# Kernel tuning notes

Measured on AMD Instinct MI355X. Metric: run time of the kernel, lower is better.

Reference implementation:

```python
import jax, jax.numpy as jnp
import numpy as np
from jax import lax

B = 16384
H = 1024   # h_dim
Z = 64     # z_dim
N = 2 * Z  # FFT length


def sample_von_mises(key, loc, kappa, rounds=32):
    """Best-Fisher rejection sampler for von Mises, vectorized, fixed rounds.
    Matches torch.distributions.VonMises.sample (non-differentiable)."""
    tau = 1.0 + jnp.sqrt(1.0 + 4.0 * kappa * kappa)
    rho = (tau - jnp.sqrt(2.0 * tau)) / (2.0 * kappa)
    r = (1.0 + rho * rho) / (2.0 * rho)

    def body(carry, k):
        theta, done = carry
        u = jax.random.uniform(k, (3,) + loc.shape, dtype=loc.dtype)
        u1, u2, u3 = u[0], u[1], u[2]
        zc = jnp.cos(jnp.pi * u1)
        f = (1.0 + r * zc) / (r + zc)
        c = kappa * (r - f)
        accept = ((c * (2.0 - c) - u2) > 0) | ((jnp.log(c / u2) + 1.0 - c) >= 0)
        prop = jnp.sign(u3 - 0.5) * jnp.arccos(jnp.clip(f, -1.0, 1.0))
        theta = jnp.where((~done) & accept, prop, theta)
        return (theta, done | accept), None

    init = (jnp.zeros_like(loc), jnp.zeros(loc.shape, bool))
    (theta, _), _ = lax.scan(body, init, jax.random.split(key, rounds))
    # shift by loc and wrap to [-pi, pi]
    return jnp.mod(theta + loc + jnp.pi, 2.0 * jnp.pi) - jnp.pi


def setup_inputs() -> dict:
    key = jax.random.key(0)
    ks = jax.random.split(key, 16)

    def lin(k, fan_in, fan_out):
        kw, kb = jax.random.split(k)
        bound = 1.0 / np.sqrt(fan_in)
        w = jax.random.uniform(kw, (fan_in, fan_out), jnp.float32, -bound, bound)
        b = jax.random.uniform(kb, (fan_out,), jnp.float32, -bound, bound)
        return w, b

    x = jax.random.uniform(ks[0], (B, 784), jnp.float32)
    enc_w1, enc_b1 = lin(ks[1], 784, 2 * H)
    enc_w2, enc_b2 = lin(ks[2], 2 * H, H)
    mu_w, mu_b = lin(ks[3], H, Z)
    conc_w, conc_b = lin(ks[4], H, 1)
    pre_w, pre_b = lin(ks[5], 4 * Z, Z)
    dec_w1, dec_b1 = lin(ks[6], Z, H)
    dec_w2, dec_b2 = lin(ks[7], H, 2 * H)
    dec_w3, dec_b3 = lin(ks[8], 2 * H, 784)
    return dict(x=x, enc_w1=enc_w1, enc_b1=enc_b1, enc_w2=enc_w2, enc_b2=enc_b2,
                mu_w=mu_w, mu_b=mu_b, conc_w=conc_w, conc_b=conc_b,
                pre_w=pre_w, pre_b=pre_b,
                dec_w1=dec_w1, dec_b1=dec_b1, dec_w2=dec_w2, dec_b2=dec_b2,
                dec_w3=dec_w3, dec_b3=dec_b3)


def reference(x, enc_w1, enc_b1, enc_w2, enc_b2, mu_w, mu_b, conc_w, conc_b,
              pre_w, pre_b, dec_w1, dec_b1, dec_w2, dec_b2, dec_w3, dec_b3):
    # ---- encode ----
    h = jax.nn.relu(x.reshape(-1, 784) @ enc_w1 + enc_b1)
    h = jax.nn.relu(h @ enc_w2 + enc_b2)
    mu = h @ mu_w + mu_b                                       # [B, Z]
    kappa = jax.nn.softplus(h @ conc_w + conc_b) + 1.0          # [B, 1]

    # ---- reparameterize: von Mises per-dim sampling (non-differentiable) ----
    kappa_full = jnp.broadcast_to(kappa, mu.shape)
    theta = sample_von_mises(jax.random.key(42),
                             lax.stop_gradient(mu),
                             lax.stop_gradient(kappa_full))     # [B, Z]
    theta = lax.stop_gradient(theta)

    # conjugate-symmetric phase spectrum: indices 0 and N/2 stay zero
    b = theta.shape[0]
    theta_s = jnp.zeros((b, N), theta.dtype)
    theta_s = theta_s.at[:, 1:Z].set(theta[:, 1:])
    theta_s = theta_s.at[:, N - Z + 1:].set(-theta[:, 1:][:, ::-1])

    z_c = jnp.fft.ifft(jnp.exp(1j * theta_s), axis=-1, norm='ortho')  # [B, N] complex
    # torch.view_as_real -> interleaved (re, im) pairs, flattened to [B, 4Z]
    z_real = jnp.stack([z_c.real, z_c.imag], axis=-1).reshape(b, -1).astype(jnp.float32)
    z = z_real @ pre_w + pre_b                                   # [B, Z]

    # ---- decode ----
    d = jax.nn.relu(z @ dec_w1 + dec_b1)
    d = jax.nn.relu(d @ dec_w2 + dec_b2)
    x_recon = d @ dec_w3 + dec_b3                                # [B, 784]
    return mu, kappa, z, x_recon
```

## Files before the change

kernel.cpp:

```cpp
#include <hip/hip_runtime.h>
#include <hip/hip_bf16.h>
#include <stdint.h>

#pragma clang fp contract(off)

#define PI_F     3.14159265358979323846f
#define TWO_PI_F 6.28318530717958647692f

typedef short short8 __attribute__((ext_vector_type(8)));
typedef float f32x4  __attribute__((ext_vector_type(4)));

__device__ __forceinline__ void tfround(uint32_t &x0, uint32_t &x1, const int r) {
  x0 += x1;
  x1 = (x1 << r) | (x1 >> (32 - r));
  x1 ^= x0;
}
__device__ __forceinline__ void threefry2x32(uint32_t k0, uint32_t k1,
                                             uint32_t &x0, uint32_t &x1) {
  uint32_t k2 = k0 ^ k1 ^ 0x1BD11BDAu;
  x0 += k0; x1 += k1;
  tfround(x0,x1,13); tfround(x0,x1,15); tfround(x0,x1,26); tfround(x0,x1,6);
  x0 += k1; x1 += k2 + 1u;
  tfround(x0,x1,17); tfround(x0,x1,29); tfround(x0,x1,16); tfround(x0,x1,24);
  x0 += k2; x1 += k0 + 2u;
  tfround(x0,x1,13); tfround(x0,x1,15); tfround(x0,x1,26); tfround(x0,x1,6);
  x0 += k0; x1 += k1 + 3u;
  tfround(x0,x1,17); tfround(x0,x1,29); tfround(x0,x1,16); tfround(x0,x1,24);
  x0 += k1; x1 += k2 + 4u;
  tfround(x0,x1,13); tfround(x0,x1,15); tfround(x0,x1,26); tfround(x0,x1,6);
  x0 += k2; x1 += k0 + 5u;
}
__device__ __forceinline__ float u01(uint32_t bits) {
  return __uint_as_float((bits >> 9) | 0x3F800000u) - 1.0f;
}
__global__ __launch_bounds__(64) void setup_keys(uint32_t* keys) {
  int r = threadIdx.x;
  if (r < 32) {
    uint32_t x0 = 0u, x1 = (uint32_t)r;
    threefry2x32(0u, 42u, x0, x1);
    keys[2 * r]     = x0;
    keys[2 * r + 1] = x1;
  }
}

__device__ __forceinline__ unsigned short bf16_rn(float v) {
  uint32_t u = __float_as_uint(v);
  return (unsigned short)((u + 0x7FFFu + ((u >> 16) & 1u)) >> 16);
}
__device__ __forceinline__ void split_bf16(float v, short &h, short &l) {
  unsigned short hb = bf16_rn(v);
  h = (short)hb;
  float hf = __uint_as_float(((uint32_t)hb) << 16);
  l = (short)bf16_rn(v - hf);
}

__global__ __launch_bounds__(256)
void split_pad(const float* __restrict__ src, short* __restrict__ dh,
               short* __restrict__ dl, int C, int Cp) {
  int r = blockIdx.x;
  for (int c = threadIdx.x; c < Cp; c += blockDim.x) {
    float v = (c < C) ? src[(size_t)r * C + c] : 0.0f;
    short h, l; split_bf16(v, h, l);
    dh[(size_t)r * Cp + c] = h;
    dl[(size_t)r * Cp + c] = l;
  }
}

__global__ __launch_bounds__(256)
void transpose_split(const float* __restrict__ src, short* __restrict__ dh,
                     short* __restrict__ dl, int K, int N, int Kp, int Np) {
  __shared__ float tile[32][33];
  int n0 = blockIdx.x * 32, k0 = blockIdx.y * 32;
  int tn = threadIdx.x & 31, tk4 = threadIdx.x >> 5;
  #pragma unroll
  for (int i = 0; i < 4; ++i) {
    int k = k0 + tk4 * 4 + i;
    float v = (k < K && (n0 + tn) < N) ? src[(size_t)k * N + n0 + tn] : 0.0f;
    tile[tk4 * 4 + i][tn] = v;
  }
  __syncthreads();
  #pragma unroll
  for (int i = 0; i < 4; ++i) {
    int n = n0 + tk4 * 4 + i;
    int k = k0 + tn;
    if (n < Np && k < Kp) {
      float v = tile[tn][tk4 * 4 + i];
      short h, l; split_bf16(v, h, l);
      dh[(size_t)n * Kp + k] = h;
      dl[(size_t)n * Kp + k] = l;
    }
  }
}

__device__ __forceinline__ void async16(void* l, const void* g) {
  __builtin_amdgcn_global_load_lds(
      (const __attribute__((address_space(1))) void*)(uintptr_t)g,
      (__attribute__((address_space(3))) void*)(uint32_t)(uintptr_t)l,
      16, 0, 0);
}

template<int RELU, int OUTMODE>
__global__ __launch_bounds__(256)
void gemm_mfma3(const short* __restrict__ Ah, const short* __restrict__ Al,
                const short* __restrict__ Bh, const short* __restrict__ Bl,
                const float* __restrict__ bias,
                float* __restrict__ Cf, short* __restrict__ Ch, short* __restrict__ Cl,
                int Kp, int NK, int Nout) {
  __shared__ short8 lds8[2048];

  int gx = gridDim.x;
  int nwg = gx * gridDim.y;
  int bid = blockIdx.y * gx + blockIdx.x;
  int cpx = nwg >> 3;
  int swz = (bid & 7) * cpx + (bid >> 3);
  int tile_x = swz % gx, tile_y = swz / gx;

  const int row0 = tile_y * 128;
  const int col0 = tile_x * 128;
  const int t = threadIdx.x;
  const int lane = t & 63, w = t >> 6;
  const int wr = w >> 1, wc = w & 1;
  const int lrow = lane & 15, lch = lane >> 4;

  f32x4 acc[4][4] = {};

  auto stage = [&](int k0) {
    #pragma unroll
    for (int q = 0; q < 8; ++q) {
      int s = q * 256 + t;
      int op = s >> 9;
      int so = s & 511;
      int chunk = so >> 7, row = so & 127;
      const short* g;
      if (op == 0)      g = Ah + (size_t)(row0 + row) * Kp + k0 + chunk * 8;
      else if (op == 1) g = Al + (size_t)(row0 + row) * Kp + k0 + chunk * 8;
      else if (op == 2) g = Bh + (size_t)(col0 + row) * Kp + k0 + chunk * 8;
      else              g = Bl + (size_t)(col0 + row) * Kp + k0 + chunk * 8;
      short8* ldst = &lds8[q * 256 + w * 64];
      async16((void*)ldst, (const void*)g);
    }
  };

  stage(0);
  for (int ks = 0; ks < NK; ++ks) {
    __syncthreads();

    short8 ah[4], al[4], bh[4], bl[4];
    #pragma unroll
    for (int mf = 0; mf < 4; ++mf) {
      int sa = lch * 128 + wr * 64 + mf * 16 + lrow;
      ah[mf] = lds8[sa];
      al[mf] = lds8[512 + sa];
    }
    #pragma unroll
    for (int nf = 0; nf < 4; ++nf) {
      int sb = lch * 128 + wc * 64 + nf * 16 + lrow;
      bh[nf] = lds8[1024 + sb];
      bl[nf] = lds8[1536 + sb];
    }
    #pragma unroll
    for (int mf = 0; mf < 4; ++mf)
      #pragma unroll
      for (int nf = 0; nf < 4; ++nf) {
        acc[mf][nf] = __builtin_amdgcn_mfma_f32_16x16x32_bf16(ah[mf], bh[nf], acc[mf][nf], 0, 0, 0);
        acc[mf][nf] = __builtin_amdgcn_mfma_f32_16x16x32_bf16(al[mf], bh[nf], acc[mf][nf], 0, 0, 0);
        acc[mf][nf] = __builtin_amdgcn_mfma_f32_16x16x32_bf16(ah[mf], bl[nf], acc[mf][nf], 0, 0, 0);
      }
    __syncthreads();
    if (ks + 1 < NK) stage((ks + 1) * 32);
  }

  #pragma unroll
  for (int mf = 0; mf < 4; ++mf)
    #pragma unroll
    for (int nf = 0; nf < 4; ++nf)
      #pragma unroll
      for (int j = 0; j < 4; ++j) {
        int grow = row0 + wr * 64 + mf * 16 + lch * 4 + j;
        int gcol = col0 + wc * 64 + nf * 16 + lrow;
        float v = acc[mf][nf][j];
        if (OUTMODE == 0) {
          if (gcol < Nout) {
            v += bias[gcol];
            if (RELU) v = fmaxf(v, 0.0f);
            Cf[(size_t)grow * Nout + gcol] = v;
          }
        } else {
          v += bias[gcol];
          if (RELU) v = fmaxf(v, 0.0f);
          short h, l; split_bf16(v, h, l);
          Ch[(size_t)grow * Nout + gcol] = h;
          Cl[(size_t)grow * Nout + gcol] = l;
        }
      }
}

#define BKK 8
__global__ __launch_bounds__(256)
void gemm_f32(const float* __restrict__ A, const float* __restrict__ W,
              const float* __restrict__ bias, float* __restrict__ C,
              int M, int N, int K, int relu) {
  __shared__ float As[BKK][128 + 4];
  __shared__ float Ws[BKK][128 + 4];
  const int t = threadIdx.x;
  const int row0 = blockIdx.y * 128;
  const int col0 = blockIdx.x * 128;
  const int tx = t & 15, ty = t >> 4;
  float acc[8][8] = {};
  for (int k0 = 0; k0 < K; k0 += BKK) {
    {
      int m = t >> 1, kk4 = (t & 1) * 4;
      const float* src = A + (size_t)(row0 + m) * K + k0 + kk4;
      float4 v = *(const float4*)src;
      As[kk4 + 0][m] = v.x; As[kk4 + 1][m] = v.y;
      As[kk4 + 2][m] = v.z; As[kk4 + 3][m] = v.w;
    }
    {
      int kk = t >> 5, c = (t & 31) * 4;
      int gc = col0 + c;
      const float* src = W + (size_t)(k0 + kk) * N + gc;
      if (gc + 3 < N) {
        float4 v = *(const float4*)src;
        Ws[kk][c] = v.x; Ws[kk][c + 1] = v.y; Ws[kk][c + 2] = v.z; Ws[kk][c + 3] = v.w;
      } else {
        #pragma unroll
        for (int j = 0; j < 4; ++j) Ws[kk][c + j] = (gc + j < N) ? src[j] : 0.0f;
      }
    }
    __syncthreads();
    #pragma unroll
    for (int kk = 0; kk < BKK; ++kk) {
      float a[8], wv[8];
      #pragma unroll
      for (int i = 0; i < 8; ++i) a[i] = As[kk][ty * 8 + i];
      #pragma unroll
      for (int j = 0; j < 8; ++j) wv[j] = Ws[kk][tx * 8 + j];
      #pragma unroll
      for (int i = 0; i < 8; ++i)
        #pragma unroll
        for (int j = 0; j < 8; ++j)
          acc[i][j] = fmaf(a[i], wv[j], acc[i][j]);
    }
    __syncthreads();
  }
  for (int i = 0; i < 8; ++i) {
    int m = row0 + ty * 8 + i;
    float* crow = C + (size_t)m * N;
    for (int j = 0; j < 8; ++j) {
      int n = col0 + tx * 8 + j;
      if (n < N) {
        float v = acc[i][j] + bias[n];
        if (relu) v = fmaxf(v, 0.0f);
        crow[n] = v;
      }
    }
  }
}

__global__ __launch_bounds__(256)
void kappa_kernel(const float* __restrict__ h, const float* __restrict__ conc_w,
                  const float* __restrict__ conc_b, float* __restrict__ kap,
                  int Brows, int K) {
  int row = blockIdx.x * 4 + (threadIdx.x >> 6);
  int lane = threadIdx.x & 63;
  if (row >= Brows) return;
  const float* hr = h + (size_t)row * K;
  float s = 0.0f;
  for (int i = lane; i < K; i += 64) s += hr[i] * conc_w[i];
  for (int off = 32; off > 0; off >>= 1) s += __shfl_down(s, off, 64);
  if (lane == 0) {
    float x = s + conc_b[0];
    float sp = fmaxf(x, 0.0f) + log1pf(expf(-fabsf(x)));
    kap[row] = sp + 1.0f;
  }
}

__device__ __forceinline__ float best_r_of(float kap) {
  float tau = 1.0f + sqrtf(1.0f + (4.0f * kap) * kap);
  float rho = (tau - sqrtf(2.0f * tau)) / (2.0f * kap);
  return (1.0f + rho * rho) / (2.0f * rho);
}
__device__ __forceinline__ void vm_step(float &theta, bool &done, float kap,
                                        float r, float u1, float u2, float u3) {
  float zc = cosf(PI_F * u1);
  float f = (1.0f + r * zc) / (r + zc);
  float c = kap * (r - f);
  bool acc1 = (c * (2.0f - c) - u2) > 0.0f;
  bool acc2 = ((logf(c / u2) + 1.0f) - c) >= 0.0f;
  if (acc1 || acc2) {
    float fcl = fminf(fmaxf(f, -1.0f), 1.0f);
    float sg = (u3 > 0.5f) ? 1.0f : ((u3 < 0.5f) ? -1.0f : 0.0f);
    theta = sg * acosf(fcl);
    done = true;
  }
}
__device__ __forceinline__ float wrap_theta(float th, float loc) {
  float y = (th + loc) + PI_F;
  float m = fmodf(y, TWO_PI_F);
  if (m < 0.0f) m += TWO_PI_F;
  return m - PI_F;
}
__global__ __launch_bounds__(256)
void vonmises_kernel(const float* __restrict__ mu, const float* __restrict__ kap,
                     const uint32_t* __restrict__ keys, float* __restrict__ theta_out) {
  __shared__ uint32_t kk[64];
  if (threadIdx.x < 64) kk[threadIdx.x] = keys[threadIdx.x];
  __syncthreads();
  uint32_t e = blockIdx.x * 256u + threadIdx.x;
  int z = (int)(e & 63u);
  bool live = (z != 0);
  float kap1 = kap[e >> 6];
  float r1 = best_r_of(kap1);
  float th1 = 0.0f;
  bool done = !live;
  for (int rd = 0; rd < 32; ++rd) {
    if (__all(done)) break;
    uint32_t K0 = kk[2 * rd], K1 = kk[2 * rd + 1];
    uint32_t a0 = 0u, a1 = e;
    uint32_t b0 = 0u, b1 = e + 1048576u;
    uint32_t c0 = 0u, c1 = e + 2097152u;
    threefry2x32(K0, K1, a0, a1);
    threefry2x32(K0, K1, b0, b1);
    threefry2x32(K0, K1, c0, c1);
    if (!done) {
      vm_step(th1, done, kap1, r1, u01(a0 ^ a1), u01(b0 ^ b1), u01(c0 ^ c1));
    }
  }
  if (live) theta_out[e] = wrap_theta(th1, mu[e]);
}

__global__ __launch_bounds__(128)
void dft_pre_kernel(const float* __restrict__ theta, const float* __restrict__ pre_w,
                    const float* __restrict__ pre_b, float* __restrict__ z_out) {
  __shared__ float ct[128], st[128], cs[64], ss[64], rez[128];
  const int b = blockIdx.x;
  const int t = threadIdx.x;
  {
    float a = (float)t * 0.015625f;
    ct[t] = cospif(a);
    st[t] = sinpif(a);
  }
  if (t >= 1 && t < 64) {
    float th = theta[(size_t)b * 64 + t];
    cs[t] = cosf(th);
    ss[t] = sinf(th);
  }
  __syncthreads();
  {
    float acc = 0.0f;
    #pragma unroll 1
    for (int k = 1; k < 64; ++k) {
      int idx = (k * t) & 127;
      acc = fmaf(cs[k], ct[idx], acc);
      acc = fmaf(-ss[k], st[idx], acc);
    }
    const float inv = 0.08838834764831845f;
    float base = (t & 1) ? 0.0f : 2.0f * inv;
    rez[t] = fmaf(2.0f * inv, acc, base);
  }
  __syncthreads();
  if (t < 64) {
    float acc = pre_b[t];
    #pragma unroll 4
    for (int n = 0; n < 128; ++n)
      acc = fmaf(rez[n], pre_w[n * 128 + t], acc);
    z_out[(size_t)b * 64 + t] = acc;
  }
}

extern "C" void kernel_launch(void* const* d_in, const int* in_sizes, int n_in,
                              void* d_out, int out_size, void* d_ws, size_t ws_size,
                              hipStream_t stream) {
  const float* x      = (const float*)d_in[0];
  const float* enc_w1 = (const float*)d_in[1];
  const float* enc_b1 = (const float*)d_in[2];
  const float* enc_w2 = (const float*)d_in[3];
  const float* enc_b2 = (const float*)d_in[4];
  const float* mu_w   = (const float*)d_in[5];
  const float* mu_b   = (const float*)d_in[6];
  const float* conc_w = (const float*)d_in[7];
  const float* conc_b = (const float*)d_in[8];
  const float* pre_w  = (const float*)d_in[9];
  const float* pre_b  = (const float*)d_in[10];
  const float* dec_w1 = (const float*)d_in[11];
  const float* dec_b1 = (const float*)d_in[12];
  const float* dec_w2 = (const float*)d_in[13];
  const float* dec_b2 = (const float*)d_in[14];
  const float* dec_w3 = (const float*)d_in[15];
  const float* dec_b3 = (const float*)d_in[16];

  float* out = (float*)d_out;
  float* mu_out  = out;
  float* kap_out = out + 1048576;
  float* z_out   = out + 1064960;
  float* xr_out  = out + 2113536;

  char* ws = (char*)d_ws;
  size_t o = 0;
  auto alloc = [&](size_t bytes) { size_t r = o; o += (bytes + 1023) & ~(size_t)1023; return r; };
  uint32_t* keys  = (uint32_t*)(ws + alloc(256));
  float*    theta = (float*)(ws + alloc(4194304));
  short* w1t_h = (short*)(ws + alloc((size_t)2048 * 800 * 2));
  short* w1t_l = (short*)(ws + alloc((size_t)2048 * 800 * 2));
  short* w2t_h = (short*)(ws + alloc((size_t)1024 * 2048 * 2));
  short* w2t_l = (short*)(ws + alloc((size_t)1024 * 2048 * 2));
  short* dw1t_h = (short*)(ws + alloc((size_t)1024 * 64 * 2));
  short* dw1t_l = (short*)(ws + alloc((size_t)1024 * 64 * 2));
  short* dw2t_h = (short*)(ws + alloc((size_t)2048 * 1024 * 2));
  short* dw2t_l = (short*)(ws + alloc((size_t)2048 * 1024 * 2));
  short* dw3t_h = (short*)(ws + alloc((size_t)896 * 2048 * 2));
  short* dw3t_l = (short*)(ws + alloc((size_t)896 * 2048 * 2));
  short* zh = (short*)(ws + alloc((size_t)16384 * 64 * 2));
  short* zl = (short*)(ws + alloc((size_t)16384 * 64 * 2));
  char* region1 = ws + alloc((size_t)2 * 16384 * 2048 * 2);
  char* region2 = ws + alloc((size_t)16384 * 1024 * 4);
  (void)ws_size;

  short* h1h = (short*)region1;
  short* h1l = (short*)(region1 + (size_t)16384 * 2048 * 2);
  short* d2h = h1h;  short* d2l = h1l;
  short* xh = (short*)region2;
  short* xl = (short*)(region2 + (size_t)16384 * 800 * 2);
  float* hbuf = (float*)region2;
  short* d1h = (short*)region2;
  short* d1l = (short*)(region2 + (size_t)16384 * 1024 * 2);

  setup_keys<<<1, 64, 0, stream>>>(keys);

  split_pad<<<16384, 256, 0, stream>>>(x, xh, xl, 784, 800);
  transpose_split<<<dim3(64, 25), 256, 0, stream>>>(enc_w1, w1t_h, w1t_l, 784, 2048, 800, 2048);
  transpose_split<<<dim3(32, 64), 256, 0, stream>>>(enc_w2, w2t_h, w2t_l, 2048, 1024, 2048, 1024);
  transpose_split<<<dim3(32, 2),  256, 0, stream>>>(dec_w1, dw1t_h, dw1t_l, 64, 1024, 64, 1024);
  transpose_split<<<dim3(64, 32), 256, 0, stream>>>(dec_w2, dw2t_h, dw2t_l, 1024, 2048, 1024, 2048);
  transpose_split<<<dim3(28, 64), 256, 0, stream>>>(dec_w3, dw3t_h, dw3t_l, 2048, 784, 2048, 896);

  gemm_mfma3<1, 1><<<dim3(16, 128), 256, 0, stream>>>(xh, xl, w1t_h, w1t_l, enc_b1,
      nullptr, h1h, h1l, 800, 25, 2048);
  gemm_mfma3<1, 0><<<dim3(8, 128), 256, 0, stream>>>(h1h, h1l, w2t_h, w2t_l, enc_b2,
      hbuf, nullptr, nullptr, 2048, 64, 1024);
  gemm_f32<<<dim3(1, 128), 256, 0, stream>>>(hbuf, mu_w, mu_b, mu_out, 16384, 64, 1024, 0);
  kappa_kernel<<<4096, 256, 0, stream>>>(hbuf, conc_w, conc_b, kap_out, 16384, 1024);

  vonmises_kernel<<<4096, 256, 0, stream>>>(mu_out, kap_out, keys, theta);
  dft_pre_kernel<<<16384, 128, 0, stream>>>(theta, pre_w, pre_b, z_out);
  split_pad<<<16384, 256, 0, stream>>>(z_out, zh, zl, 64, 64);

  gemm_mfma3<1, 1><<<dim3(8, 128), 256, 0, stream>>>(zh, zl, dw1t_h, dw1t_l, dec_b1,
      nullptr, d1h, d1l, 64, 2, 1024);
  gemm_mfma3<1, 1><<<dim3(16, 128), 256, 0, stream>>>(d1h, d1l, dw2t_h, dw2t_l, dec_b2,
      nullptr, d2h, d2l, 1024, 32, 2048);
  gemm_mfma3<0, 0><<<dim3(7, 128), 256, 0, stream>>>(d2h, d2l, dw3t_h, dw3t_l, dec_b3,
      xr_out, nullptr, nullptr, 2048, 64, 784);
}
```

Before: 1.604 ms.

## Replace 128x128 split-bf16 GEMM with 256x256 double-buffered 512-thread kernel

Replaces the 128x128-tile, 256-thread GEMM with a 256x256-tile, 512-thread kernel. It double-buffers 64 KB LDS stages, uses XOR-swizzled LDS layout and interleaves async global-to-LDS prefetch with MFMA groups under raised s_setprio. The three split-precision products (hi*hi, lo*hi, hi*lo) become a sequence of K tiles instead of being fused per step. This targets higher arithmetic intensity and hides load latency. In exchange it pads K and N more (832, 1024), leaves fewer workgroups per GPU, and uses 128 KB LDS, which limits occupancy to one block per CU.

```diff
diff --git a/kernel.cpp b/kernel.cpp
--- a/kernel.cpp
+++ b/kernel.cpp
@@ -9,6 +9,10 @@
 
 typedef short short8 __attribute__((ext_vector_type(8)));
 typedef float f32x4  __attribute__((ext_vector_type(4)));
+
+template<int V> struct IC { static constexpr int v = V; };
+
+#define BARRIER() do { asm volatile("" ::: "memory"); __builtin_amdgcn_s_barrier(); asm volatile("" ::: "memory"); } while(0)
 
 __device__ __forceinline__ void tfround(uint32_t &x0, uint32_t &x1, const int r) {
   x0 += x1;
@@ -100,13 +104,13 @@
 }
 
 template<int RELU, int OUTMODE>
-__global__ __launch_bounds__(256)
-void gemm_mfma3(const short* __restrict__ Ah, const short* __restrict__ Al,
-                const short* __restrict__ Bh, const short* __restrict__ Bl,
-                const float* __restrict__ bias,
-                float* __restrict__ Cf, short* __restrict__ Ch, short* __restrict__ Cl,
-                int Kp, int NK, int Nout) {
-  __shared__ short8 lds8[2048];
+__global__ __launch_bounds__(512)
+void gemm256(const short* __restrict__ Ah, const short* __restrict__ Al,
+             const short* __restrict__ Bh, const short* __restrict__ Bl,
+             const float* __restrict__ bias,
+             float* __restrict__ Cf, short* __restrict__ Ch, short* __restrict__ Cl,
+             int Kp, int KTP, int Nout) {
+  __shared__ __align__(1024) char smem[131072];
 
   int gx = gridDim.x;
   int nwg = gx * gridDim.y;
@@ -115,70 +119,116 @@
   int swz = (bid & 7) * cpx + (bid >> 3);
   int tile_x = swz % gx, tile_y = swz / gx;
 
-  const int row0 = tile_y * 128;
-  const int col0 = tile_x * 128;
-  const int t = threadIdx.x;
-  const int lane = t & 63, w = t >> 6;
-  const int wr = w >> 1, wc = w & 1;
+  const int trow0 = tile_y * 256;
+  const int col0  = tile_x * 256;
+  const int t512 = threadIdx.x;
+  const int lane = t512 & 63, w = t512 >> 6;
+  const int wm = w >> 2, wn = w & 3;
   const int lrow = lane & 15, lch = lane >> 4;
-
-  f32x4 acc[4][4] = {};
-
-  auto stage = [&](int k0) {
+  const int rB0 = (wn & 1) * 64;
+  const int sbit = ((lane >> 2) & 1) << 5;
+  const int srow = w * 8 + (lane >> 3);
+  const int scbs = ((lane & 7) * 16) ^ (((lane >> 5) & 1) << 5);
+
+  const int NT = 3 * KTP;
+  f32x4 acc[8][4] = {};
+
+  auto stage_chunk = [&](int tile, int c) {
+    int p, kk;
+    if (tile >= 2 * KTP)      { p = 2; kk = tile - 2 * KTP; }
+    else if (tile >= KTP)     { p = 1; kk = tile - KTP; }
+    else                      { p = 0; kk = tile; }
+    const char* Abase = (const char*)((p == 1) ? Al : Ah);
+    const char* Bbase = (const char*)((p == 2) ? Bl : Bh);
+    int quarter = c >> 1, round = c & 1;
+    int rloc = round * 64 + srow;
+    const char* src;
+    if (quarter < 2)
+      src = Abase + ((size_t)(trow0 + quarter * 128 + rloc) * (size_t)Kp) * 2 + kk * 128 + scbs;
+    else
+      src = Bbase + ((size_t)(col0 + (quarter - 2) * 128 + rloc) * (size_t)Kp) * 2 + kk * 128 + scbs;
+    char* dst = smem + (tile & 1) * 65536 + quarter * 16384 + round * 8192 + w * 1024;
+    async16((void*)dst, (const void*)src);
+  };
+
+  #pragma unroll
+  for (int c = 0; c < 8; ++c) stage_chunk(0, c);
+
+  for (int t = 0; t < NT; ++t) {
+    const int tn = t + 1;
+    const bool pf = tn < NT;
+    const char* lA = smem + (t & 1) * 65536 + wm * 16384;
+    const char* lB = smem + (t & 1) * 65536 + 32768 + (wn >> 1) * 16384;
+
+    if (pf) {
+      stage_chunk(tn, 0); stage_chunk(tn, 1);
+      asm volatile("s_waitcnt vmcnt(2)" ::: "memory");
+    } else {
+      asm volatile("s_waitcnt vmcnt(0)" ::: "memory");
+    }
+    BARRIER();
+
+    auto grp = [&](auto icmq) {
+      constexpr int MQ = decltype(icmq)::v;
+      if (MQ == 1 && pf) { stage_chunk(tn, 4); stage_chunk(tn, 5); }
+      short8 af[4][2], bf[2][2];
+      #pragma unroll
+      for (int mf = 0; mf < 4; ++mf)
+        #pragma unroll
+        for (int ks = 0; ks < 2; ++ks) {
+          int r = MQ * 64 + mf * 16 + lrow;
+          af[mf][ks] = *(const short8*)(lA + r * 128 + ((ks * 64 + lch * 16) ^ sbit));
+        }
+      #pragma unroll
+      for (int nf = 0; nf < 2; ++nf)
+        #pragma unroll
+        for (int ks = 0; ks < 2; ++ks) {
+          int r = rB0 + nf * 16 + lrow;
+          bf[nf][ks] = *(const short8*)(lB + r * 128 + ((ks * 64 + lch * 16) ^ sbit));
+        }
+      __builtin_amdgcn_s_setprio(1);
+      #pragma unroll
+      for (int ks = 0; ks < 2; ++ks)
+        #pragma unroll
+        for (int mf = 0; mf < 4; ++mf)
+          #pragma unroll
+          for (int nf = 0; nf < 2; ++nf)
+            acc[MQ*4+mf][nf] = __builtin_amdgcn_mfma_f32_16x16x32_bf16(
+                af[mf][ks], bf[nf][ks], acc[MQ*4+mf][nf], 0, 0, 0);
+      __builtin_amdgcn_s_setprio(0);
+      if (pf) { stage_chunk(tn, MQ*4+2); stage_chunk(tn, MQ*4+3); }
+      #pragma unroll
+      for (int nf = 0; nf < 2; ++nf)
+        #pragma unroll
+        for (int ks = 0; ks < 2; ++ks) {
+          int r = rB0 + 32 + nf * 16 + lrow;
+          bf[nf][ks] = *(const short8*)(lB + r * 128 + ((ks * 64 + lch * 16) ^ sbit));
+        }
+      __builtin_amdgcn_s_setprio(1);
+      #pragma unroll
+      for (int ks = 0; ks < 2; ++ks)
+        #pragma unroll
+        for (int mf = 0; mf < 4; ++mf)
+          #pragma unroll
+          for (int nf = 0; nf < 2; ++nf)
+            acc[MQ*4+mf][2+nf] = __builtin_amdgcn_mfma_f32_16x16x32_bf16(
+                af[mf][ks], bf[nf][ks], acc[MQ*4+mf][2+nf], 0, 0, 0);
+      __builtin_amdgcn_s_setprio(0);
+    };
+    grp(IC<0>{});
+    grp(IC<1>{});
+    BARRIER();
+  }
+
+  #pragma unroll
+  for (int m = 0; m < 8; ++m)
     #pragma unroll
-    for (int q = 0; q < 8; ++q) {
-      int s = q * 256 + t;
-      int op = s >> 9;
-      int so = s & 511;
-      int chunk = so >> 7, row = so & 127;
-      const short* g;
-      if (op == 0)      g = Ah + (size_t)(row0 + row) * Kp + k0 + chunk * 8;
-      else if (op == 1) g = Al + (size_t)(row0 + row) * Kp + k0 + chunk * 8;
-      else if (op == 2) g = Bh + (size_t)(col0 + row) * Kp + k0 + chunk * 8;
-      else              g = Bl + (size_t)(col0 + row) * Kp + k0 + chunk * 8;
-      short8* ldst = &lds8[q * 256 + w * 64];
-      async16((void*)ldst, (const void*)g);
-    }
-  };
-
-  stage(0);
-  for (int ks = 0; ks < NK; ++ks) {
-    __syncthreads();
-
-    short8 ah[4], al[4], bh[4], bl[4];
-    #pragma unroll
-    for (int mf = 0; mf < 4; ++mf) {
-      int sa = lch * 128 + wr * 64 + mf * 16 + lrow;
-      ah[mf] = lds8[sa];
-      al[mf] = lds8[512 + sa];
-    }
-    #pragma unroll
-    for (int nf = 0; nf < 4; ++nf) {
-      int sb = lch * 128 + wc * 64 + nf * 16 + lrow;
-      bh[nf] = lds8[1024 + sb];
-      bl[nf] = lds8[1536 + sb];
-    }
-    #pragma unroll
-    for (int mf = 0; mf < 4; ++mf)
-      #pragma unroll
-      for (int nf = 0; nf < 4; ++nf) {
-        acc[mf][nf] = __builtin_amdgcn_mfma_f32_16x16x32_bf16(ah[mf], bh[nf], acc[mf][nf], 0, 0, 0);
-        acc[mf][nf] = __builtin_amdgcn_mfma_f32_16x16x32_bf16(al[mf], bh[nf], acc[mf][nf], 0, 0, 0);
-        acc[mf][nf] = __builtin_amdgcn_mfma_f32_16x16x32_bf16(ah[mf], bl[nf], acc[mf][nf], 0, 0, 0);
-      }
-    __syncthreads();
-    if (ks + 1 < NK) stage((ks + 1) * 32);
-  }
-
-  #pragma unroll
-  for (int mf = 0; mf < 4; ++mf)
-    #pragma unroll
-    for (int nf = 0; nf < 4; ++nf)
+    for (int n = 0; n < 4; ++n)
       #pragma unroll
       for (int j = 0; j < 4; ++j) {
-        int grow = row0 + wr * 64 + mf * 16 + lch * 4 + j;
-        int gcol = col0 + wc * 64 + nf * 16 + lrow;
-        float v = acc[mf][nf][j];
+        int grow = trow0 + wm * 128 + m * 16 + lch * 4 + j;
+        int gcol = col0 + wn * 64 + n * 16 + lrow;
+        float v = acc[m][n][j];
         if (OUTMODE == 0) {
           if (gcol < Nout) {
             v += bias[gcol];
@@ -400,16 +450,16 @@
   auto alloc = [&](size_t bytes) { size_t r = o; o += (bytes + 1023) & ~(size_t)1023; return r; };
   uint32_t* keys  = (uint32_t*)(ws + alloc(256));
   float*    theta = (float*)(ws + alloc(4194304));
-  short* w1t_h = (short*)(ws + alloc((size_t)2048 * 800 * 2));
-  short* w1t_l = (short*)(ws + alloc((size_t)2048 * 800 * 2));
+  short* w1t_h = (short*)(ws + alloc((size_t)2048 * 832 * 2));
+  short* w1t_l = (short*)(ws + alloc((size_t)2048 * 832 * 2));
   short* w2t_h = (short*)(ws + alloc((size_t)1024 * 2048 * 2));
   short* w2t_l = (short*)(ws + alloc((size_t)1024 * 2048 * 2));
   short* dw1t_h = (short*)(ws + alloc((size_t)1024 * 64 * 2));
   short* dw1t_l = (short*)(ws + alloc((size_t)1024 * 64 * 2));
   short* dw2t_h = (short*)(ws + alloc((size_t)2048 * 1024 * 2));
   short* dw2t_l = (short*)(ws + alloc((size_t)2048 * 1024 * 2));
-  short* dw3t_h = (short*)(ws + alloc((size_t)896 * 2048 * 2));
-  short* dw3t_l = (short*)(ws + alloc((size_t)896 * 2048 * 2));
+  short* dw3t_h = (short*)(ws + alloc((size_t)1024 * 2048 * 2));
+  short* dw3t_l = (short*)(ws + alloc((size_t)1024 * 2048 * 2));
   short* zh = (short*)(ws + alloc((size_t)16384 * 64 * 2));
   short* zl = (short*)(ws + alloc((size_t)16384 * 64 * 2));
   char* region1 = ws + alloc((size_t)2 * 16384 * 2048 * 2);
@@ -420,24 +470,24 @@
   short* h1l = (short*)(region1 + (size_t)16384 * 2048 * 2);
   short* d2h = h1h;  short* d2l = h1l;
   short* xh = (short*)region2;
-  short* xl = (short*)(region2 + (size_t)16384 * 800 * 2);
+  short* xl = (short*)(region2 + (size_t)16384 * 832 * 2);
   float* hbuf = (float*)region2;
   short* d1h = (short*)region2;
   short* d1l = (short*)(region2 + (size_t)16384 * 1024 * 2);
 
   setup_keys<<<1, 64, 0, stream>>>(keys);
 
-  split_pad<<<16384, 256, 0, stream>>>(x, xh, xl, 784, 800);
-  transpose_split<<<dim3(64, 25), 256, 0, stream>>>(enc_w1, w1t_h, w1t_l, 784, 2048, 800, 2048);
+  split_pad<<<16384, 256, 0, stream>>>(x, xh, xl, 784, 832);
+  transpose_split<<<dim3(64, 26), 256, 0, stream>>>(enc_w1, w1t_h, w1t_l, 784, 2048, 832, 2048);
   transpose_split<<<dim3(32, 64), 256, 0, stream>>>(enc_w2, w2t_h, w2t_l, 2048, 1024, 2048, 1024);
   transpose_split<<<dim3(32, 2),  256, 0, stream>>>(dec_w1, dw1t_h, dw1t_l, 64, 1024, 64, 1024);
   transpose_split<<<dim3(64, 32), 256, 0, stream>>>(dec_w2, dw2t_h, dw2t_l, 1024, 2048, 1024, 2048);
-  transpose_split<<<dim3(28, 64), 256, 0, stream>>>(dec_w3, dw3t_h, dw3t_l, 2048, 784, 2048, 896);
-
-  gemm_mfma3<1, 1><<<dim3(16, 128), 256, 0, stream>>>(xh, xl, w1t_h, w1t_l, enc_b1,
-      nullptr, h1h, h1l, 800, 25, 2048);
-  gemm_mfma3<1, 0><<<dim3(8, 128), 256, 0, stream>>>(h1h, h1l, w2t_h, w2t_l, enc_b2,
-      hbuf, nullptr, nullptr, 2048, 64, 1024);
+  transpose_split<<<dim3(32, 64), 256, 0, stream>>>(dec_w3, dw3t_h, dw3t_l, 2048, 784, 2048, 1024);
+
+  gemm256<1, 1><<<dim3(8, 64), 512, 0, stream>>>(xh, xl, w1t_h, w1t_l, enc_b1,
+      nullptr, h1h, h1l, 832, 13, 2048);
+  gemm256<1, 0><<<dim3(4, 64), 512, 0, stream>>>(h1h, h1l, w2t_h, w2t_l, enc_b2,
+      hbuf, nullptr, nullptr, 2048, 32, 1024);
   gemm_f32<<<dim3(1, 128), 256, 0, stream>>>(hbuf, mu_w, mu_b, mu_out, 16384, 64, 1024, 0);
   kappa_kernel<<<4096, 256, 0, stream>>>(hbuf, conc_w, conc_b, kap_out, 16384, 1024);
 
@@ -445,10 +495,10 @@
   dft_pre_kernel<<<16384, 128, 0, stream>>>(theta, pre_w, pre_b, z_out);
   split_pad<<<16384, 256, 0, stream>>>(z_out, zh, zl, 64, 64);
 
-  gemm_mfma3<1, 1><<<dim3(8, 128), 256, 0, stream>>>(zh, zl, dw1t_h, dw1t_l, dec_b1,
-      nullptr, d1h, d1l, 64, 2, 1024);
-  gemm_mfma3<1, 1><<<dim3(16, 128), 256, 0, stream>>>(d1h, d1l, dw2t_h, dw2t_l, dec_b2,
-      nullptr, d2h, d2l, 1024, 32, 2048);
-  gemm_mfma3<0, 0><<<dim3(7, 128), 256, 0, stream>>>(d2h, d2l, dw3t_h, dw3t_l, dec_b3,
-      xr_out, nullptr, nullptr, 2048, 64, 784);
-}
+  gemm256<1, 1><<<dim3(4, 64), 512, 0, stream>>>(zh, zl, dw1t_h, dw1t_l, dec_b1,
+      nullptr, d1h, d1l, 64, 1, 1024);
+  gemm256<1, 1><<<dim3(8, 64), 512, 0, stream>>>(d1h, d1l, dw2t_h, dw2t_l, dec_b2,
+      nullptr, d2h, d2l, 1024, 16, 2048);
+  gemm256<0, 0><<<dim3(4, 64), 512, 0, stream>>>(d2h, d2l, dw3t_h, dw3t_l, dec_b3,
+      xr_out, nullptr, nullptr, 2048, 32, 784);
+}
```

Result: slower. 2.278 ms (+42.0%).
